# Kernel tuning notes

Hardware: AMD Instinct MI355X
Metric: run time of the kernel (lower is better)

## Reference

```python
import jax, jax.numpy as jnp
import numpy as np

N_EMBED = 1024
SEQ_LEN = 2048
BATCH = 4


def setup_inputs() -> dict:
    key = jax.random.key(0)
    ks = jax.random.split(key, 9)
    E = N_EMBED
    x = jax.random.normal(ks[0], (BATCH, SEQ_LEN, E), dtype=jnp.float32)
    s = 0.02
    return {
        "x": x,
        "Wq": jax.random.normal(ks[1], (E, E), dtype=jnp.float32) * s,
        "bq": jnp.zeros((E,), dtype=jnp.float32),
        "Wk": jax.random.normal(ks[2], (E, E), dtype=jnp.float32) * s,
        "bk": jnp.zeros((E,), dtype=jnp.float32),
        "Wv": jax.random.normal(ks[3], (E, E), dtype=jnp.float32) * s,
        "bv": jnp.zeros((E,), dtype=jnp.float32),
        "Wp": jax.random.normal(ks[4], (E, E), dtype=jnp.float32) * s,
        "bp": jnp.zeros((E,), dtype=jnp.float32),
    }


def reference(x, Wq, bq, Wk, bk, Wv, bv, Wp, bp):
    # x: [B, S, E]. Original torch code unpacks (B, C, N) = x.shape and
    # scales by sqrt(C) == sqrt(seq_len)  (a bug we faithfully replicate).
    B, S, E = x.shape
    q = jnp.einsum('bse,fe->bsf', x, Wq) + bq
    k = jnp.einsum('bse,fe->bsf', x, Wk) + bk
    v = jnp.einsum('bse,fe->bsf', x, Wv) + bv
    scale = 1.0 / jnp.sqrt(jnp.asarray(S, dtype=x.dtype))
    scores = jnp.einsum('bqe,bke->bqk', q, k) * scale  # [B, S, S]
    # NOTE: original calls masked_fill (non-inplace) and discards the result,
    # so NO causal mask is actually applied. Replicate that: plain softmax.
    w = jax.nn.softmax(scores, axis=-1)
    o = jnp.einsum('bqk,bke->bqe', w, v)
    out = jnp.einsum('bse,fe->bsf', o, Wp) + bp
    return out
```

## Files before the change

kernel.cpp:

```cpp
#include <hip/hip_runtime.h>


typedef __bf16 bf16x8 __attribute__((ext_vector_type(8)));
typedef float  f32x4  __attribute__((ext_vector_type(4)));
typedef unsigned short u16x8 __attribute__((ext_vector_type(8)));

__device__ __forceinline__ float bf2f(unsigned short u) {
  return __uint_as_float(((unsigned int)u) << 16);
}
__device__ __forceinline__ unsigned short f2bf(float f) {
  unsigned int u = __float_as_uint(f);
  return (unsigned short)((u + 0x7fffu + ((u >> 16) & 1u)) >> 16);
}
__device__ __forceinline__ void gload16(const void* g, void* l) {
  __builtin_amdgcn_global_load_lds(
      (const __attribute__((address_space(1))) void*)g,
      (__attribute__((address_space(3))) void*)l, 16, 0, 0);
}

template <int EPI>
__device__ __forceinline__ void gemm32_core(
    char* lds, int nwg, int base,
    const unsigned short* __restrict__ A, const unsigned short* __restrict__ B,
    void* __restrict__ C, const float* __restrict__ bias,
    int K, long long sA, long long sB, long long sC,
    int nbm, int nbn, int ldc) {
  char* ldsA = lds;
  char* ldsB = lds + 32768;

  int id = (int)blockIdx.x - base;
  id = (id & 7) * (nwg >> 3) + (id >> 3);
  const int nbmn = nbm * nbn;
  const int bz = id / nbmn;
  const int rem = id - bz * nbmn;
  const int bm = rem / nbn;
  const int bn = rem - bm * nbn;
  const int gm0 = bm * 256, gn0 = bn * 128;

  const unsigned short* Ag = A + (size_t)bz * sA;
  const unsigned short* Bg = B + (size_t)bz * sB;

  const int tid = threadIdx.x;
  const int w = tid >> 6, l = tid & 63;
  const int wr = w >> 1, wc = w & 1;
  const int lr = l & 15;
  const int rchunk = ((l >> 4) ^ ((lr >> 1) & 3)) << 4;

  const int srow = tid >> 2;
  const int sbo  = (((tid & 3) ^ ((tid >> 3) & 3)) << 4);
  const int sdst = tid * 16;

#define STG32_A(bufsel, ktile)                                                 \
  do {                                                                         \
    char* _d = ldsA + (bufsel) * 16384 + sdst;                                 \
    const char* _s0 = (const char*)(Ag + (size_t)(gm0 + srow) * K) +           \
                      (size_t)(ktile) * 64 + sbo;                              \
    const char* _s1 = (const char*)(Ag + (size_t)(gm0 + 128 + srow) * K) +     \
                      (size_t)(ktile) * 64 + sbo;                              \
    gload16(_s0, _d);                                                          \
    gload16(_s1, _d + 8192);                                                   \
  } while (0)
#define STG32_B(bufsel, ktile)                                                 \
  do {                                                                         \
    const char* _s = (const char*)(Bg + (size_t)(gn0 + srow) * K) +            \
                     (size_t)(ktile) * 64 + sbo;                               \
    gload16(_s, ldsB + (bufsel) * 8192 + sdst);                                \
  } while (0)

#define RD32_A(dst, m)                                                         \
  dst = *(const bf16x8*)(Abuf + (wr * 64 + (m) * 16 + lr) * 64 + rchunk)
#define RD32_B(dst, n)                                                         \
  dst = *(const bf16x8*)(Bbuf + (wc * 64 + (n) * 16 + lr) * 64 + rchunk)

  f32x4 acc[4][4];
#pragma unroll
  for (int i = 0; i < 4; ++i)
#pragma unroll
    for (int j = 0; j < 4; ++j) acc[i][j] = (f32x4){0.f, 0.f, 0.f, 0.f};

  const int nt = K >> 5;

  STG32_A(0, 0); STG32_B(0, 0);
  asm volatile("s_waitcnt vmcnt(0)" ::: "memory");
  __builtin_amdgcn_s_barrier();

  for (int t = 0; t < nt; ++t) {
    const int cur = t & 1;
    char* Abuf = ldsA + cur * 16384;
    char* Bbuf = ldsB + cur * 8192;
    const bool pf = (t + 1 < nt);

    if (pf) { STG32_A(cur ^ 1, t + 1); STG32_B(cur ^ 1, t + 1); }

    bf16x8 av[4], bv[4];
#pragma unroll
    for (int m = 0; m < 4; ++m) RD32_A(av[m], m);
#pragma unroll
    for (int n = 0; n < 4; ++n) RD32_B(bv[n], n);
    asm volatile("s_waitcnt lgkmcnt(0)" ::: "memory");
    __builtin_amdgcn_sched_barrier(0);
    __builtin_amdgcn_s_setprio(1);
#pragma unroll
    for (int m = 0; m < 4; ++m)
#pragma unroll
      for (int n = 0; n < 4; ++n)
        acc[m][n] = __builtin_amdgcn_mfma_f32_16x16x32_bf16(av[m], bv[n],
                                                            acc[m][n], 0, 0, 0);
    __builtin_amdgcn_s_setprio(0);
    if (pf) { asm volatile("s_waitcnt vmcnt(0)" ::: "memory"); }
    __builtin_amdgcn_s_barrier();
  }

  const int cr = (l >> 4) * 4;
  const int cc = l & 15;
  unsigned short* Cp = (unsigned short*)C + (size_t)bz * sC;
#pragma unroll
  for (int m = 0; m < 4; ++m) {
    const int row = gm0 + wr * 64 + m * 16 + cr;
#pragma unroll
    for (int n = 0; n < 4; ++n) {
      const int col = gn0 + wc * 64 + n * 16 + cc;
      f32x4 a = acc[m][n];
#pragma unroll
      for (int j = 0; j < 4; ++j) {
        float v;
        if constexpr (EPI == 4) v = a[j] + bias[row + j];
        else                    v = a[j] + bias[col];
        Cp[(size_t)(row + j) * ldc + col] = f2bf(v);
      }
    }
  }
#undef STG32_A
#undef STG32_B
#undef RD32_A
#undef RD32_B
}

template <int EPI>
__device__ __forceinline__ void gemm_core(
    char* lds, int nwg, int base,
    const unsigned short* __restrict__ A, const unsigned short* __restrict__ B,
    void* __restrict__ C, const float* __restrict__ bias,
    const float* __restrict__ rowsum,
    int K, long long sA, long long sB, long long sC,
    int nbm, int nbn, int ldc, float scale) {
  char* ldsA = lds;
  char* ldsB = lds + 98304;

  int id = (int)blockIdx.x - base;
  id = (id & 7) * (nwg >> 3) + (id >> 3);
  const int nbmn = nbm * nbn;
  const int bz = id / nbmn;
  const int rem = id - bz * nbmn;
  const int bm = rem / nbn;
  const int bn = rem - bm * nbn;
  const int gm0 = bm * 256, gn0 = bn * 128;

  const unsigned short* Ag = A + (size_t)bz * sA;
  const unsigned short* Bg = B + (size_t)bz * sB;

  const int tid = threadIdx.x;
  const int w = tid >> 6, l = tid & 63;
  const int wr = w >> 1, wc = w & 1;
  const int lr = l & 15;
  const int lk16 = (l >> 4) * 16;
  const int swz = (lr & 7) << 4;

  const int srow = tid >> 3;
  const int sbo  = ((tid & 7) * 16) ^ ((srow & 7) << 4);
  const int sdst = tid * 16;

#define STG_A2(region, ktile, half)                                            \
  do {                                                                         \
    const char* _b =                                                           \
        (const char*)(Ag + (size_t)(gm0 + srow + (half) * 128) * K) +          \
        (size_t)(ktile) * 128 + sbo;                                           \
    const size_t _rk = (size_t)64 * K * 2;                                     \
    gload16(_b,       (region) + (half) * 16384 + sdst);                       \
    gload16(_b + _rk, (region) + (half) * 16384 + 8192 + sdst);                \
  } while (0)
#define STG_B(region, ktile)                                                   \
  do {                                                                         \
    const char* _b = (const char*)(Bg + (size_t)(gn0 + srow) * K) +            \
                     (size_t)(ktile) * 128 + sbo;                              \
    const size_t _rk = (size_t)64 * K * 2;                                     \
    gload16(_b,       (region) + sdst);                                        \
    gload16(_b + _rk, (region) + 8192 + sdst);                                 \
  } while (0)

#define RD_A(dst, m, kh)                                                       \
  dst = *(const bf16x8*)(Abuf + (wr * 64 + (m) * 16 + lr) * 128 +              \
                         ((lk16 + (kh) * 64) ^ swz))
#define RD_B(dst, n, kh)                                                       \
  dst = *(const bf16x8*)(Bbuf + (wc * 64 + (n) * 16 + lr) * 128 +              \
                         ((lk16 + (kh) * 64) ^ swz))

#define LGKM_PIN()                                          \
  asm volatile("s_waitcnt lgkmcnt(0)" ::: "memory");        \
  __builtin_amdgcn_sched_barrier(0)

#define MFMA8(mi0, mi1)                                                        \
  __builtin_amdgcn_s_setprio(1);                                               \
  _Pragma("unroll")                                                            \
  for (int n = 0; n < 4; ++n) {                                                \
    acc[mi0][n] = __builtin_amdgcn_mfma_f32_16x16x32_bf16(a0, bfr[n],          \
                                                          acc[mi0][n], 0,0,0); \
    acc[mi1][n] = __builtin_amdgcn_mfma_f32_16x16x32_bf16(a1, bfr[n],          \
                                                          acc[mi1][n], 0,0,0); \
  }                                                                            \
  __builtin_amdgcn_s_setprio(0)

  f32x4 acc[4][4];
#pragma unroll
  for (int i = 0; i < 4; ++i)
#pragma unroll
    for (int j = 0; j < 4; ++j) acc[i][j] = (f32x4){0.f, 0.f, 0.f, 0.f};

  const int nt = K >> 6;

  STG_B(ldsB, 0); STG_A2(ldsA, 0, 0); STG_A2(ldsA, 0, 1);
  if (nt > 1) {
    STG_B(ldsB + 16384, 1);
    STG_A2(ldsA + 32768, 1, 0); STG_A2(ldsA + 32768, 1, 1);
  }
  if (nt > 1) { asm volatile("s_waitcnt vmcnt(6)" ::: "memory"); }
  else        { asm volatile("s_waitcnt vmcnt(0)" ::: "memory"); }
  __builtin_amdgcn_s_barrier();

  int cur = 0;
  for (int t = 0; t < nt; ++t) {
    char* Abuf = ldsA + cur * 32768;
    char* Bbuf = ldsB + cur * 16384;
    const int nx2 = (cur + 2 >= 3) ? cur - 1 : cur + 2;
    const bool pf = (t + 2 < nt);

    bf16x8 a0, a1, bfr[4];
    RD_A(a0, 0, 0); RD_A(a1, 1, 0);
#pragma unroll
    for (int n = 0; n < 4; ++n) RD_B(bfr[n], n, 0);
    if (pf) STG_B(ldsB + nx2 * 16384, t + 2);
    __builtin_amdgcn_s_barrier();
    LGKM_PIN();
    MFMA8(0, 1);
    __builtin_amdgcn_s_barrier();

    RD_A(a0, 2, 0); RD_A(a1, 3, 0);
    if (pf) STG_A2(ldsA + nx2 * 32768, t + 2, 0);
    __builtin_amdgcn_s_barrier();
    LGKM_PIN();
    MFMA8(2, 3);
    __builtin_amdgcn_s_barrier();

    RD_A(a0, 0, 1); RD_A(a1, 1, 1);
#pragma unroll
    for (int n = 0; n < 4; ++n) RD_B(bfr[n], n, 1);
    if (pf) STG_A2(ldsA + nx2 * 32768, t + 2, 1);
    __builtin_amdgcn_s_barrier();
    LGKM_PIN();
    MFMA8(0, 1);
    __builtin_amdgcn_s_barrier();

    RD_A(a0, 2, 1); RD_A(a1, 3, 1);
    __builtin_amdgcn_s_barrier();
    LGKM_PIN();
    MFMA8(2, 3);
    if (pf)              { asm volatile("s_waitcnt vmcnt(6)" ::: "memory"); }
    else if (t + 1 < nt) { asm volatile("s_waitcnt vmcnt(0)" ::: "memory"); }
    __builtin_amdgcn_s_barrier();

    cur = (cur + 1 >= 3) ? 0 : cur + 1;
  }

  const int cr = (l >> 4) * 4;
  const int cc = l & 15;
#pragma unroll
  for (int m = 0; m < 4; ++m) {
    const int row = gm0 + wr * 64 + m * 16 + cr;
    if constexpr (EPI == 3) {
      const float* rs = rowsum + bz * 2048 + row;
      const f32x4 rv = *(const f32x4*)rs;
      f32x4 inv;
#pragma unroll
      for (int j = 0; j < 4; ++j) inv[j] = 1.0f / rv[j];
      float* Cp = (float*)C + (size_t)bz * sC;
#pragma unroll
      for (int n = 0; n < 4; ++n) {
        const int col = gn0 + wc * 64 + n * 16 + cc;
        const float b = bias[col];
        f32x4 a = acc[m][n];
#pragma unroll
        for (int j = 0; j < 4; ++j)
          Cp[(size_t)(row + j) * ldc + col] = a[j] * inv[j] + b;
      }
    } else {
      unsigned short* Cp = (unsigned short*)C + (size_t)bz * sC;
#pragma unroll
      for (int n = 0; n < 4; ++n) {
        const int col = gn0 + wc * 64 + n * 16 + cc;
        f32x4 a = acc[m][n];
#pragma unroll
        for (int j = 0; j < 4; ++j) {
          float v;
          if constexpr (EPI == 1)      v = a[j] * scale;
          else if constexpr (EPI == 4) v = a[j] + bias[row + j];
          else                         v = a[j] + bias[col];
          Cp[(size_t)(row + j) * ldc + col] = f2bf(v);
        }
      }
    }
  }
#undef STG_A2
#undef STG_B
#undef RD_A
#undef RD_B
#undef LGKM_PIN
#undef MFMA8
}

__global__ __launch_bounds__(256) void prep1(
    const float* __restrict__ wq, const float* __restrict__ wk,
    const float* __restrict__ wv, const float* __restrict__ wp,
    unsigned short* __restrict__ qt, unsigned short* __restrict__ kt,
    unsigned short* __restrict__ vt, unsigned short* __restrict__ wp_bf,
    float* __restrict__ rowsum) {
  const int tid = threadIdx.x;
  if (blockIdx.x >= 1280) {
    const int i = ((blockIdx.x - 1280) * 256 + tid) * 8;
    *(f32x4*)(rowsum + i) = (f32x4){0.f, 0.f, 0.f, 0.f};
    *(f32x4*)(rowsum + i + 4) = (f32x4){0.f, 0.f, 0.f, 0.f};
    return;
  }
  if (blockIdx.x >= 768) {
    const int i = ((blockIdx.x - 768) * 256 + tid) * 8;
    f32x4 a = *(const f32x4*)(wp + i);
    f32x4 b = *(const f32x4*)(wp + i + 4);
    u16x8 o;
    o[0] = f2bf(a[0]); o[1] = f2bf(a[1]); o[2] = f2bf(a[2]); o[3] = f2bf(a[3]);
    o[4] = f2bf(b[0]); o[5] = f2bf(b[1]); o[6] = f2bf(b[2]); o[7] = f2bf(b[3]);
    *(u16x8*)(wp_bf + i) = o;
    return;
  }
  const float* in;
  unsigned short* out;
  int b = blockIdx.x;
  if (b < 256)      { in = wq; out = qt; }
  else if (b < 512) { in = wk; out = kt; b -= 256; }
  else              { in = wv; out = vt; b -= 512; }
  const int r0 = (b >> 4) * 64, c0 = (b & 15) * 64;
  __shared__ unsigned short t[64][72];
  const int rr = tid >> 4;
  const int cc4 = (tid & 15) * 4;
#pragma unroll
  for (int p = 0; p < 4; ++p) {
    const int r = rr + p * 16;
    f32x4 v = *(const f32x4*)(in + (size_t)(r0 + r) * 1024 + c0 + cc4);
    t[cc4 + 0][r] = f2bf(v[0]);
    t[cc4 + 1][r] = f2bf(v[1]);
    t[cc4 + 2][r] = f2bf(v[2]);
    t[cc4 + 3][r] = f2bf(v[3]);
  }
  __syncthreads();
  const int wr_ = tid >> 3;
  const int wc8 = (tid & 7) * 8;
#pragma unroll
  for (int p = 0; p < 2; ++p) {
    const int c = wr_ + p * 32;
    u16x8 o;
#pragma unroll
    for (int j = 0; j < 8; ++j) o[j] = t[c][wc8 + j];
    *(u16x8*)(out + (size_t)(c0 + c) * 1024 + r0 + wc8) = o;
  }
}

__global__ __launch_bounds__(512) void prep2(
    const unsigned short* __restrict__ WkT, const unsigned short* __restrict__ WqT,
    const unsigned short* __restrict__ Wp_bf, const unsigned short* __restrict__ WvT,
    unsigned short* __restrict__ HT, unsigned short* __restrict__ G,
    const float* __restrict__ x, unsigned short* __restrict__ x_bf,
    const float* __restrict__ bq, const float* __restrict__ Wk,
    const float* __restrict__ Wp, const float* __restrict__ bv,
    float* __restrict__ c1, float* __restrict__ cv, float scale) {
  __shared__ char lds[147456];
  const int bid = (int)blockIdx.x;
  const int tid = threadIdx.x;
  if (bid < 32) {
    gemm_core<1>(lds, 32, 0, WkT, WqT, HT, nullptr, nullptr,
                 1024, 0, 0, 0, 4, 8, 1024, scale);
  } else if (bid < 64) {
    gemm_core<1>(lds, 32, 32, Wp_bf, WvT, G, nullptr, nullptr,
                 1024, 0, 0, 0, 4, 8, 1024, 1.0f);
  } else if (bid < 224) {
    for (int u = (bid - 64) * 512 + tid; u < 1048576; u += 160 * 512) {
      const int i = u * 8;
      f32x4 a = *(const f32x4*)(x + i);
      f32x4 b = *(const f32x4*)(x + i + 4);
      u16x8 o;
      o[0] = f2bf(a[0]); o[1] = f2bf(a[1]); o[2] = f2bf(a[2]); o[3] = f2bf(a[3]);
      o[4] = f2bf(b[0]); o[5] = f2bf(b[1]); o[6] = f2bf(b[2]); o[7] = f2bf(b[3]);
      *(u16x8*)(x_bf + i) = o;
    }
  } else if (bid < 226) {
    const int e = (bid - 224) * 512 + tid;
    float acc = 0.f;
    for (int f = 0; f < 1024; ++f) acc += bq[f] * Wk[(size_t)f * 1024 + e];
    c1[e] = acc * scale;
  } else {
    const int l = tid & 63;
    for (int e = (bid - 226) * 8 + (tid >> 6); e < 1024; e += 240) {
      float acc = 0.f;
#pragma unroll
      for (int f = l; f < 1024; f += 64) acc += Wp[(size_t)e * 1024 + f] * bv[f];
#pragma unroll
      for (int i = 1; i < 64; i <<= 1) acc += __shfl_xor(acc, i, 64);
      if (l == 0) cv[e] = acc;
    }
  }
}

__global__ __launch_bounds__(512, 4) void gmid(
    const unsigned short* x, const unsigned short* HT, unsigned short* R,
    const float* c1, const unsigned short* G, unsigned short* VWt,
    const float* cv) {
  __shared__ char lds[49152];
  if (blockIdx.x < 256)
    gemm32_core<5>(lds, 256, 0, x, HT, R, c1,
                   1024, 0, 0, 0, 32, 8, 1024);
  else
    gemm32_core<4>(lds, 256, 256, G, x, VWt, cv,
                   1024, 0, 2097152, 2097152, 4, 16, 2048);
}

__global__ __launch_bounds__(512) void gout(
    const unsigned short* E, const unsigned short* VWt, float* out,
    const float* bp, const float* rowsum) {
  __shared__ char lds[147456];
  gemm_core<3>(lds, 256, 0, E, VWt, out, bp, rowsum,
               2048, 4194304, 2097152, 2097152, 8, 8, 1024, 0.f);
}

__global__ __launch_bounds__(512) void gsco8(
    const unsigned short* __restrict__ A, const unsigned short* __restrict__ B,
    unsigned short* __restrict__ C, float* __restrict__ rowsum,
    int K, long long sA, long long sB, long long sC, int nbm, int nbn) {
  __shared__ char lds[131072];
  char* ldsA = lds;
  char* ldsB = lds + 65536;

  const int nwg = (int)gridDim.x;
  int id = (int)blockIdx.x;
  id = (id & 7) * (nwg >> 3) + (id >> 3);
  const int nbmn = nbm * nbn;
  const int bz = id / nbmn;
  const int rem = id - bz * nbmn;
  const int bm = rem / nbn;
  const int bn = rem - bm * nbn;
  const int gm0 = bm * 256, gn0 = bn * 256;

  const unsigned short* Ag = A + (size_t)bz * sA;
  const unsigned short* Bg = B + (size_t)bz * sB;

  const int tid = threadIdx.x;
  const int w = tid >> 6, l = tid & 63;
  const int wr = w >> 2, wc = w & 3;
  const int lr = l & 15;
  const int lk16 = (l >> 4) * 16;
  const int swz = (lr & 7) << 4;

  const int srow0 = (tid * 16) >> 7;
  const int srow1 = srow0 + 64;
  const int sbo   = ((tid * 16) & 127) ^ ((srow0 & 7) << 4);
  const int sdst0 = tid * 16;
  const int sdst1 = tid * 16 + 8192;

#define STAGE(gbase, grow0, region, ktile)                                     \
  do {                                                                         \
    const char* _s0 =                                                          \
        (const char*)((gbase) + (size_t)((grow0) + srow0) * K) +               \
        (ktile) * 128 + sbo;                                                   \
    const char* _s1 =                                                          \
        (const char*)((gbase) + (size_t)((grow0) + srow1) * K) +               \
        (ktile) * 128 + sbo;                                                   \
    gload16(_s0, (region) + sdst0);                                            \
    gload16(_s1, (region) + sdst1);                                            \
  } while (0)

#define RDA(dst, m, kh) \
  dst = *(const bf16x8*)(Areg + ((m) * 16 + lr) * 128 + ((lk16 + (kh) * 64) ^ swz))
#define RDB(dst, n, kh) \
  dst = *(const bf16x8*)(Breg + (((wc & 1) * 64 + (n) * 16 + lr) * 128) + ((lk16 + (kh) * 64) ^ swz))

  f32x4 acc[8][4];
#pragma unroll
  for (int i = 0; i < 8; ++i)
#pragma unroll
    for (int j = 0; j < 4; ++j) acc[i][j] = (f32x4){0.f, 0.f, 0.f, 0.f};

  bf16x8 af[4][2], bf_[4][2];

#define MM(mi, ai, n)                                                          \
  acc[mi][n] = __builtin_amdgcn_mfma_f32_16x16x32_bf16(af[ai][0], bf_[n][0],   \
                                                       acc[mi][n], 0, 0, 0);   \
  acc[mi][n] = __builtin_amdgcn_mfma_f32_16x16x32_bf16(af[ai][1], bf_[n][1],   \
                                                       acc[mi][n], 0, 0, 0)

#define LGKM_PIN()                                          \
  asm volatile("s_waitcnt lgkmcnt(0)" ::: "memory");        \
  __builtin_amdgcn_sched_barrier(0)

  const int nt = K >> 6;

  STAGE(Bg, gn0,       ldsB + 0,     0);
  STAGE(Bg, gn0 + 128, ldsB + 16384, 0);
  STAGE(Ag, gm0,       ldsA + 0,     0);
  STAGE(Ag, gm0 + 128, ldsA + 16384, 0);
  STAGE(Bg, gn0,       ldsB + 32768,         1);
  STAGE(Bg, gn0 + 128, ldsB + 32768 + 16384, 1);
  STAGE(Ag, gm0,       ldsA + 32768,         1);
  asm volatile("s_waitcnt vmcnt(6)" ::: "memory");
  __builtin_amdgcn_s_barrier();

  for (int t = 0; t < nt; ++t) {
    const int cur = t & 1;
    char* Areg  = ldsA + cur * 32768 + wr * 16384;
    char* Breg  = ldsB + cur * 32768 + (wc >> 1) * 16384;
    char* Anext = ldsA + (cur ^ 1) * 32768;
    char* Acur2 = ldsA + cur * 32768;
    char* Bcur2 = ldsB + cur * 32768;

#pragma unroll
    for (int m = 0; m < 4; ++m) { RDA(af[m][0], m, 0); RDA(af[m][1], m, 1); }
#pragma unroll
    for (int n = 0; n < 2; ++n) { RDB(bf_[n][0], n, 0); RDB(bf_[n][1], n, 1); }
    if (wc < 2) {
#pragma unroll
      for (int n = 2; n < 4; ++n) { RDB(bf_[n][0], n, 0); RDB(bf_[n][1], n, 1); }
    }
    if (t + 1 < nt) STAGE(Ag, gm0 + 128, Anext + 16384, t + 1);
    __builtin_amdgcn_s_barrier();
    LGKM_PIN();
    __builtin_amdgcn_s_setprio(1);
    MM(0, 0, 0); MM(0, 0, 1); MM(1, 1, 0); MM(1, 1, 1);
    MM(2, 2, 0); MM(2, 2, 1); MM(3, 3, 0); MM(3, 3, 1);
    __builtin_amdgcn_s_setprio(0);
    __builtin_amdgcn_s_barrier();

    if (wc >= 2) {
#pragma unroll
      for (int n = 2; n < 4; ++n) { RDB(bf_[n][0], n, 0); RDB(bf_[n][1], n, 1); }
    }
    if (t + 2 < nt) STAGE(Bg, gn0, Bcur2, t + 2);
    __builtin_amdgcn_s_barrier();
    LGKM_PIN();
    __builtin_amdgcn_s_setprio(1);
    MM(0, 0, 2); MM(0, 0, 3); MM(1, 1, 2); MM(1, 1, 3);
    MM(2, 2, 2); MM(2, 2, 3); MM(3, 3, 2); MM(3, 3, 3);
    __builtin_amdgcn_s_setprio(0);
    __builtin_amdgcn_s_barrier();

#pragma unroll
    for (int m = 0; m < 4; ++m) { RDA(af[m][0], m + 4, 0); RDA(af[m][1], m + 4, 1); }
    if (t + 2 < nt) STAGE(Bg, gn0 + 128, Bcur2 + 16384, t + 2);
    __builtin_amdgcn_s_barrier();
    LGKM_PIN();
    __builtin_amdgcn_s_setprio(1);
    MM(4, 0, 0); MM(4, 0, 1); MM(5, 1, 0); MM(5, 1, 1);
    MM(6, 2, 0); MM(6, 2, 1); MM(7, 3, 0); MM(7, 3, 1);
    __builtin_amdgcn_s_setprio(0);
    __builtin_amdgcn_s_barrier();

    if (t + 2 < nt) STAGE(Ag, gm0, Acur2, t + 2);
    __builtin_amdgcn_s_barrier();
    __builtin_amdgcn_s_setprio(1);
    MM(4, 0, 2); MM(4, 0, 3); MM(5, 1, 2); MM(5, 1, 3);
    MM(6, 2, 2); MM(6, 2, 3); MM(7, 3, 2); MM(7, 3, 3);
    __builtin_amdgcn_s_setprio(0);
    if (t + 2 < nt) {
      asm volatile("s_waitcnt vmcnt(6)" ::: "memory");
    } else {
      asm volatile("s_waitcnt vmcnt(0)" ::: "memory");
    }
    __builtin_amdgcn_s_barrier();
  }

  const int cr = (l >> 4) * 4;
  const int cc = l & 15;
  unsigned short* Cp = C + (size_t)bz * sC;
#pragma unroll
  for (int m = 0; m < 8; ++m) {
    const int row = gm0 + wr * 128 + m * 16 + cr;
    float psum[4] = {0.f, 0.f, 0.f, 0.f};
#pragma unroll
    for (int n = 0; n < 4; ++n) {
      const int col = gn0 + wc * 64 + n * 16 + cc;
      f32x4 a = acc[m][n];
#pragma unroll
      for (int j = 0; j < 4; ++j) {
        const unsigned short us = f2bf(exp2f(a[j]));
        Cp[(size_t)(row + j) * 2048 + col] = us;
        psum[j] += bf2f(us);
      }
    }
#pragma unroll
    for (int j = 0; j < 4; ++j) {
#pragma unroll
      for (int i = 1; i < 16; i <<= 1) psum[j] += __shfl_xor(psum[j], i, 16);
      if ((l & 15) == 0) atomicAdd(rowsum + bz * 2048 + row + j, psum[j]);
    }
  }
#undef STAGE
#undef RDA
#undef RDB
#undef MM
#undef LGKM_PIN
}

extern "C" void kernel_launch(void* const* d_in, const int* in_sizes, int n_in,
                              void* d_out, int out_size, void* d_ws, size_t ws_size,
                              hipStream_t stream) {
  const float* x  = (const float*)d_in[0];
  const float* Wq = (const float*)d_in[1];
  const float* bq = (const float*)d_in[2];
  const float* Wk = (const float*)d_in[3];
  const float* bk = (const float*)d_in[4];  (void)bk;
  const float* Wv = (const float*)d_in[5];
  const float* bv = (const float*)d_in[6];
  const float* Wp = (const float*)d_in[7];
  const float* bp = (const float*)d_in[8];
  float* out = (float*)d_out;

  char* ws = (char*)d_ws;
  unsigned short* x_bf  = (unsigned short*)(ws);
  unsigned short* Wp_bf = (unsigned short*)(ws + (16ull << 20));
  unsigned short* WqT   = (unsigned short*)(ws + (18ull << 20));
  unsigned short* WkT   = (unsigned short*)(ws + (20ull << 20));
  unsigned short* WvT   = (unsigned short*)(ws + (22ull << 20));
  unsigned short* HT    = (unsigned short*)(ws + (24ull << 20));
  unsigned short* G     = (unsigned short*)(ws + (26ull << 20));
  float*          c1    = (float*)(ws + (28ull << 20));
  float*          cv    = (float*)(ws + (28ull << 20) + 65536);
  unsigned short* R     = (unsigned short*)(ws + (32ull << 20));
  unsigned short* VWt   = (unsigned short*)(ws + (48ull << 20));
  unsigned short* Em    = (unsigned short*)(ws + (64ull << 20));
  float*          rowsum = (float*)(ws + (96ull << 20));

  const float scale_ht = 0.022097086912079608f * 1.4426950408889634f;

  prep1<<<1284, 256, 0, stream>>>(Wq, Wk, Wv, Wp, WqT, WkT, WvT, Wp_bf, rowsum);
  prep2<<<256, 512, 0, stream>>>(WkT, WqT, Wp_bf, WvT, HT, G,
                                 x, x_bf, bq, Wk, Wp, bv, c1, cv, scale_ht);
  gmid<<<512, 512, 0, stream>>>(x_bf, HT, R, c1, G, VWt, cv);
  gsco8<<<256, 512, 0, stream>>>(R, x_bf, Em, rowsum,
                                 1024, 2097152, 2097152, 4194304, 8, 8);
  gout<<<256, 512, 0, stream>>>(Em, VWt, out, bp, rowsum);
}
```

Baseline: 164.6 us.

## Compute softmax row sums via MFMA with ones in output GEMM, drop atomics

Removes the rowsum buffer, its zeroing in prep1, and the shuffle-reduce plus atomicAdd in the score kernel's epilogue. Instead, the output GEMM accumulates row sums of the exp matrix by issuing extra MFMAs against a ones vector alongside the main MFMAs. This trades global atomics and an extra buffer round trip for a small number of additional MFMA instructions per K step. The change also narrows the non-EPI3 epilogue to the scale-only path.

```diff
diff --git a/kernel.cpp b/kernel.cpp
--- a/kernel.cpp
+++ b/kernel.cpp
@@ -141,7 +141,6 @@
     char* lds, int nwg, int base,
     const unsigned short* __restrict__ A, const unsigned short* __restrict__ B,
     void* __restrict__ C, const float* __restrict__ bias,
-    const float* __restrict__ rowsum,
     int K, long long sA, long long sB, long long sC,
     int nbm, int nbn, int ldc, float scale) {
   char* ldsA = lds;
@@ -210,11 +209,30 @@
   }                                                                            \
   __builtin_amdgcn_s_setprio(0)
 
+#define RSUM(mi0, mi1)                                                         \
+  if constexpr (EPI == 3) {                                                    \
+    acc_rs[mi0] = __builtin_amdgcn_mfma_f32_16x16x32_bf16(a0, onesB,           \
+                                                          acc_rs[mi0], 0,0,0); \
+    acc_rs[mi1] = __builtin_amdgcn_mfma_f32_16x16x32_bf16(a1, onesB,           \
+                                                          acc_rs[mi1], 0,0,0); \
+  }
+
   f32x4 acc[4][4];
 #pragma unroll
   for (int i = 0; i < 4; ++i)
 #pragma unroll
     for (int j = 0; j < 4; ++j) acc[i][j] = (f32x4){0.f, 0.f, 0.f, 0.f};
+
+  f32x4 acc_rs[4];
+  bf16x8 onesB;
+  if constexpr (EPI == 3) {
+    u16x8 ou;
+#pragma unroll
+    for (int j = 0; j < 8; ++j) ou[j] = 0x3F80;
+    onesB = *(bf16x8*)&ou;
+#pragma unroll
+    for (int i = 0; i < 4; ++i) acc_rs[i] = (f32x4){0.f, 0.f, 0.f, 0.f};
+  }
 
   const int nt = K >> 6;
 
@@ -242,6 +260,7 @@
     __builtin_amdgcn_s_barrier();
     LGKM_PIN();
     MFMA8(0, 1);
+    RSUM(0, 1)
     __builtin_amdgcn_s_barrier();
 
     RD_A(a0, 2, 0); RD_A(a1, 3, 0);
@@ -249,6 +268,7 @@
     __builtin_amdgcn_s_barrier();
     LGKM_PIN();
     MFMA8(2, 3);
+    RSUM(2, 3)
     __builtin_amdgcn_s_barrier();
 
     RD_A(a0, 0, 1); RD_A(a1, 1, 1);
@@ -258,12 +278,14 @@
     __builtin_amdgcn_s_barrier();
     LGKM_PIN();
     MFMA8(0, 1);
+    RSUM(0, 1)
     __builtin_amdgcn_s_barrier();
 
     RD_A(a0, 2, 1); RD_A(a1, 3, 1);
     __builtin_amdgcn_s_barrier();
     LGKM_PIN();
     MFMA8(2, 3);
+    RSUM(2, 3)
     if (pf)              { asm volatile("s_waitcnt vmcnt(6)" ::: "memory"); }
     else if (t + 1 < nt) { asm volatile("s_waitcnt vmcnt(0)" ::: "memory"); }
     __builtin_amdgcn_s_barrier();
@@ -277,11 +299,9 @@
   for (int m = 0; m < 4; ++m) {
     const int row = gm0 + wr * 64 + m * 16 + cr;
     if constexpr (EPI == 3) {
-      const float* rs = rowsum + bz * 2048 + row;
-      const f32x4 rv = *(const f32x4*)rs;
       f32x4 inv;
 #pragma unroll
-      for (int j = 0; j < 4; ++j) inv[j] = 1.0f / rv[j];
+      for (int j = 0; j < 4; ++j) inv[j] = 1.0f / acc_rs[m][j];
       float* Cp = (float*)C + (size_t)bz * sC;
 #pragma unroll
       for (int n = 0; n < 4; ++n) {
@@ -299,13 +319,8 @@
         const int col = gn0 + wc * 64 + n * 16 + cc;
         f32x4 a = acc[m][n];
 #pragma unroll
-        for (int j = 0; j < 4; ++j) {
-          float v;
-          if constexpr (EPI == 1)      v = a[j] * scale;
-          else if constexpr (EPI == 4) v = a[j] + bias[row + j];
-          else                         v = a[j] + bias[col];
-          Cp[(size_t)(row + j) * ldc + col] = f2bf(v);
-        }
+        for (int j = 0; j < 4; ++j)
+          Cp[(size_t)(row + j) * ldc + col] = f2bf(a[j] * scale);
       }
     }
   }
@@ -315,21 +330,15 @@
 #undef RD_B
 #undef LGKM_PIN
 #undef MFMA8
+#undef RSUM
 }
 
 __global__ __launch_bounds__(256) void prep1(
     const float* __restrict__ wq, const float* __restrict__ wk,
     const float* __restrict__ wv, const float* __restrict__ wp,
     unsigned short* __restrict__ qt, unsigned short* __restrict__ kt,
-    unsigned short* __restrict__ vt, unsigned short* __restrict__ wp_bf,
-    float* __restrict__ rowsum) {
+    unsigned short* __restrict__ vt, unsigned short* __restrict__ wp_bf) {
   const int tid = threadIdx.x;
-  if (blockIdx.x >= 1280) {
-    const int i = ((blockIdx.x - 1280) * 256 + tid) * 8;
-    *(f32x4*)(rowsum + i) = (f32x4){0.f, 0.f, 0.f, 0.f};
-    *(f32x4*)(rowsum + i + 4) = (f32x4){0.f, 0.f, 0.f, 0.f};
-    return;
-  }
   if (blockIdx.x >= 768) {
     const int i = ((blockIdx.x - 768) * 256 + tid) * 8;
     f32x4 a = *(const f32x4*)(wp + i);
@@ -384,10 +393,10 @@
   const int bid = (int)blockIdx.x;
   const int tid = threadIdx.x;
   if (bid < 32) {
-    gemm_core<1>(lds, 32, 0, WkT, WqT, HT, nullptr, nullptr,
+    gemm_core<1>(lds, 32, 0, WkT, WqT, HT, nullptr,
                  1024, 0, 0, 0, 4, 8, 1024, scale);
   } else if (bid < 64) {
-    gemm_core<1>(lds, 32, 32, Wp_bf, WvT, G, nullptr, nullptr,
+    gemm_core<1>(lds, 32, 32, Wp_bf, WvT, G, nullptr,
                  1024, 0, 0, 0, 4, 8, 1024, 1.0f);
   } else if (bid < 224) {
     for (int u = (bid - 64) * 512 + tid; u < 1048576; u += 160 * 512) {
@@ -432,15 +441,15 @@
 
 __global__ __launch_bounds__(512) void gout(
     const unsigned short* E, const unsigned short* VWt, float* out,
-    const float* bp, const float* rowsum) {
+    const float* bp) {
   __shared__ char lds[147456];
-  gemm_core<3>(lds, 256, 0, E, VWt, out, bp, rowsum,
+  gemm_core<3>(lds, 256, 0, E, VWt, out, bp,
                2048, 4194304, 2097152, 2097152, 8, 8, 1024, 0.f);
 }
 
 __global__ __launch_bounds__(512) void gsco8(
     const unsigned short* __restrict__ A, const unsigned short* __restrict__ B,
-    unsigned short* __restrict__ C, float* __restrict__ rowsum,
+    unsigned short* __restrict__ C,
     int K, long long sA, long long sB, long long sC, int nbm, int nbn) {
   __shared__ char lds[131072];
   char* ldsA = lds;
@@ -588,23 +597,13 @@
 #pragma unroll
   for (int m = 0; m < 8; ++m) {
     const int row = gm0 + wr * 128 + m * 16 + cr;
-    float psum[4] = {0.f, 0.f, 0.f, 0.f};
 #pragma unroll
     for (int n = 0; n < 4; ++n) {
       const int col = gn0 + wc * 64 + n * 16 + cc;
       f32x4 a = acc[m][n];
 #pragma unroll
-      for (int j = 0; j < 4; ++j) {
-        const unsigned short us = f2bf(exp2f(a[j]));
-        Cp[(size_t)(row + j) * 2048 + col] = us;
-        psum[j] += bf2f(us);
-      }
-    }
-#pragma unroll
-    for (int j = 0; j < 4; ++j) {
-#pragma unroll
-      for (int i = 1; i < 16; i <<= 1) psum[j] += __shfl_xor(psum[j], i, 16);
-      if ((l & 15) == 0) atomicAdd(rowsum + bz * 2048 + row + j, psum[j]);
+      for (int j = 0; j < 4; ++j)
+        Cp[(size_t)(row + j) * 2048 + col] = f2bf(exp2f(a[j]));
     }
   }
 #undef STAGE
@@ -641,15 +640,14 @@
   unsigned short* R     = (unsigned short*)(ws + (32ull << 20));
   unsigned short* VWt   = (unsigned short*)(ws + (48ull << 20));
   unsigned short* Em    = (unsigned short*)(ws + (64ull << 20));
-  float*          rowsum = (float*)(ws + (96ull << 20));
 
   const float scale_ht = 0.022097086912079608f * 1.4426950408889634f;
 
-  prep1<<<1284, 256, 0, stream>>>(Wq, Wk, Wv, Wp, WqT, WkT, WvT, Wp_bf, rowsum);
+  prep1<<<1280, 256, 0, stream>>>(Wq, Wk, Wv, Wp, WqT, WkT, WvT, Wp_bf);
   prep2<<<256, 512, 0, stream>>>(WkT, WqT, Wp_bf, WvT, HT, G,
                                  x, x_bf, bq, Wk, Wp, bv, c1, cv, scale_ht);
   gmid<<<512, 512, 0, stream>>>(x_bf, HT, R, c1, G, VWt, cv);
-  gsco8<<<256, 512, 0, stream>>>(R, x_bf, Em, rowsum,
+  gsco8<<<256, 512, 0, stream>>>(R, x_bf, Em,
                                  1024, 2097152, 2097152, 4194304, 8, 8);
-  gout<<<256, 512, 0, stream>>>(Em, VWt, out, bp, rowsum);
-}
+  gout<<<256, 512, 0, stream>>>(Em, VWt, out, bp);
+}
```

After: 157.9 us. 4.1% less time.
